# Kernel optimization log

Hardware: AMD Instinct MI355X
Metric: run time of the kernel (lower is better)

## Reference

```python
import jax, jax.numpy as jnp
import numpy as np

STRIDE = (2, 2)
PADDING = (1, 1)
DILATION = (1, 1)
KERNEL = (3, 3)


def _out_hw(h_in, w_in):
    h_out = (h_in + 2 * PADDING[0] - DILATION[0] * (KERNEL[0] - 1) - 1) // STRIDE[0] + 1
    w_out = (w_in + 2 * PADDING[1] - DILATION[1] * (KERNEL[1] - 1) - 1) // STRIDE[1] + 1
    return h_out, w_out


def _stride_permutation(h_out, w_out):
    # Single-shot multiplexing row permutation (mirrors _get_stride_permutation).
    s_h, s_w = STRIDE
    if s_h == 1 and s_w == 1:
        return np.arange(h_out * w_out)
    perm = []
    for si in range(s_h):
        for sj in range(s_w):
            for i in range((h_out + s_h - 1) // s_h):
                ai = i * s_h + si
                if ai >= h_out:
                    continue
                for j in range((w_out + s_w - 1) // s_w):
                    aj = j * s_w + sj
                    if aj >= w_out:
                        continue
                    perm.append(ai * w_out + aj)
    return np.asarray(perm, dtype=np.int32)


def setup_inputs() -> dict:
    key = jax.random.key(0)
    kx, kw, kb = jax.random.split(key, 3)
    x = jax.random.normal(kx, (16, 256, 64, 64), dtype=jnp.float32)
    weight = jax.random.normal(kw, (256, 256, 3, 3), dtype=jnp.float32)
    bias = jax.random.normal(kb, (256,), dtype=jnp.float32)
    return {"x": x, "weight": weight, "bias": bias}


def reference(x, weight, bias):
    # Toeplitz matrix-vector product == grouped strided conv.
    out = jax.lax.conv_general_dilated(
        x, weight,
        window_strides=STRIDE,
        padding=[(PADDING[0], PADDING[0]), (PADDING[1], PADDING[1])],
        rhs_dilation=DILATION,
        dimension_numbers=("NCHW", "OIHW", "NCHW"),
        feature_group_count=1,
    )  # [B, Cout, h_out, w_out]
    b, c, h_out, w_out = out.shape
    perm = jnp.asarray(_stride_permutation(h_out, w_out))
    flat = out.reshape(b, c, h_out * w_out)
    # permuted[new_idx] = flat[perm[new_idx]] (single-shot stride multiplexing)
    permuted = flat[:, :, perm]
    return permuted + bias[None, :, None]
```

## Files before the change

kernel.cpp:

```cpp
#include <hip/hip_runtime.h>
#include <cstdint>

typedef __attribute__((ext_vector_type(8))) __bf16 bf16x8;
typedef __attribute__((ext_vector_type(4))) float f32x4;
typedef __attribute__((ext_vector_type(4))) uint32_t u32x4;

#define NB   16
#define CIN  256
#define COUT 256
#define HP   66
#define WP   66
#define KTOT 2304
#define XPB  (HP*WP*256)
#define XPAD_ELEMS (NB*XPB)

__device__ __forceinline__ uint16_t f2bf(float f) {
  uint32_t u = __builtin_bit_cast(uint32_t, f);
  u = (u + 0x7FFFu + ((u >> 16) & 1u)) >> 16;
  return (uint16_t)u;
}

__global__ void prep_kernel(const float* __restrict__ x, const float* __restrict__ w,
                            uint16_t* __restrict__ xpad, uint16_t* __restrict__ bw) {
  const int bid = blockIdx.x;
  const int tid = threadIdx.x;
  if (bid < 2048) {
    const int lane = tid & 63;
    const int wvi = tid >> 6;
    const int chalf = bid & 1;
    const int h = (bid >> 1) & 63;
    const int b = bid >> 7;
    const int c0 = chalf * 128 + wvi * 32;
    const float* src = x + ((size_t)(b * 256 + c0) * 64 + h) * 64 + lane;
    uint16_t* dst = xpad + ((size_t)(b * HP + h + 1) * WP + lane + 1) * 256 + c0;
    #pragma unroll
    for (int g = 0; g < 4; ++g) {
      u32x4 d;
      #pragma unroll
      for (int k = 0; k < 4; ++k) {
        const float v0 = src[(size_t)(g * 8 + 2 * k + 0) * 4096];
        const float v1 = src[(size_t)(g * 8 + 2 * k + 1) * 4096];
        d[k] = (uint32_t)f2bf(v0) | ((uint32_t)f2bf(v1) << 16);
      }
      *(u32x4*)(dst + g * 8) = d;
    }
  } else if (bid < 3088) {
    const int idx = (bid - 2048) * 256 + tid;
    const int b = idx / 16640;
    const int r = idx - b * 16640;
    uint64_t* base = (uint64_t*)(xpad + (size_t)b * XPB);
    int off;
    if (r < 4224) {
      off = r;
    } else if (r < 8448) {
      off = 274560 + (r - 4224);
    } else if (r < 12544) {
      const int i = r - 8448;
      off = (1 + (i >> 6)) * 4224 + (i & 63);
    } else {
      const int i = r - 12544;
      off = (1 + (i >> 6)) * 4224 + 4160 + (i & 63);
    }
    base[off] = 0;
  } else {
    const int gid = (bid - 3088) * 256 + tid;
    const int co = gid / 288;
    const int r = gid - co * 288;
    const int tap = r >> 5;
    const int ci0 = (r & 31) * 8;
    u32x4 d;
    #pragma unroll
    for (int k = 0; k < 4; ++k) {
      const float v0 = w[((co * 256 + ci0 + 2 * k + 0) * 9) + tap];
      const float v1 = w[((co * 256 + ci0 + 2 * k + 1) * 9) + tap];
      d[k] = (uint32_t)f2bf(v0) | ((uint32_t)f2bf(v1) << 16);
    }
    *(u32x4*)(bw + co * KTOT + tap * 256 + ci0) = d;
  }
}

__device__ __forceinline__ void gl_lds16(const void* g, void* l) {
  __builtin_amdgcn_global_load_lds(
      (__attribute__((address_space(1))) void*)(uintptr_t)g,
      (__attribute__((address_space(3))) void*)(uint32_t)(uintptr_t)l,
      16, 0, 0);
}

__global__ __launch_bounds__(256, 2) void gemm_kernel(
    const uint16_t* __restrict__ xpad, const uint16_t* __restrict__ bw,
    const float* __restrict__ bias, float* __restrict__ out) {
  __shared__ uint16_t lA[2][128 * 64];
  __shared__ uint16_t lB[2][64 * 64];
  const int tid = threadIdx.x;
  const int wv = tid >> 6, lane = tid & 63;
  const int quad = lane >> 4, l15 = lane & 15, l7 = lane & 7;

  const int xcd = blockIdx.x & 7;
  const int grp = blockIdx.x >> 3;
  const int mtile = (xcd << 4) + (grp >> 2);
  const int ntile = grp & 3;
  const int n0 = ntile * 64;
  const int m0 = mtile * 128;
  const int bidx = m0 >> 10;
  const int q0 = m0 & 1023;

  int a_goff[4];
  #pragma unroll
  for (int t = 0; t < 4; ++t) {
    const int slot = t * 256 + tid;
    const int row = slot >> 3;
    const int kc = (slot & 7) ^ (row & 7);
    const int p = q0 + row;
    const int oh = 2 * ((p >> 4) & 15) + ((p >> 9) & 1);
    const int ow = 2 * (p & 15) + ((p >> 8) & 1);
    a_goff[t] = ((bidx * HP + 2 * oh) * WP + 2 * ow) * 256 + kc * 8;
  }
  int b_goff[2];
  #pragma unroll
  for (int t = 0; t < 2; ++t) {
    const int slot = t * 256 + tid;
    const int n = slot >> 3;
    const int kc = (slot & 7) ^ (n & 7);
    b_goff[t] = (n0 + n) * KTOT + kc * 8;
  }

  int aoff[2][2], boff[4][2];
  #pragma unroll
  for (int r = 0; r < 2; ++r)
    #pragma unroll
    for (int s = 0; s < 2; ++s)
      aoff[r][s] = (wv * 32 + r * 16 + l15) * 128 + (((s * 4 + quad) ^ l7) * 16);
  #pragma unroll
  for (int c = 0; c < 4; ++c)
    #pragma unroll
    for (int s = 0; s < 2; ++s)
      boff[c][s] = (c * 16 + l15) * 128 + (((s * 4 + quad) ^ l7) * 16);

  f32x4 acc[2][4];
  #pragma unroll
  for (int r = 0; r < 2; ++r)
    #pragma unroll
    for (int c = 0; c < 4; ++c)
      acc[r][c] = (f32x4){0.f, 0.f, 0.f, 0.f};

  auto stage = [&](int it, int buf) {
    const int tap = it >> 2;
    const int kh = tap / 3, kw = tap - kh * 3;
    const int ci0 = (it & 3) << 6;
    const uint16_t* aptr = xpad + (kh * WP + kw) * 256 + ci0;
    const uint16_t* bptr = bw + tap * 256 + ci0;
    char* la = (char*)&lA[buf][0];
    char* lb = (char*)&lB[buf][0];
    #pragma unroll
    for (int t = 0; t < 4; ++t)
      gl_lds16(aptr + a_goff[t], la + (t * 256 + wv * 64) * 16);
    #pragma unroll
    for (int t = 0; t < 2; ++t)
      gl_lds16(bptr + b_goff[t], lb + (t * 256 + wv * 64) * 16);
  };

  stage(0, 0);
  int buf = 0;
  for (int it = 0; it < 36; ++it) {
    __syncthreads();
    if (it < 35) stage(it + 1, buf ^ 1);
    const char* la = (const char*)&lA[buf][0];
    const char* lb = (const char*)&lB[buf][0];
    #pragma unroll
    for (int s = 0; s < 2; ++s) {
      bf16x8 af[2], bfr[4];
      #pragma unroll
      for (int r = 0; r < 2; ++r) af[r] = *(const bf16x8*)(la + aoff[r][s]);
      #pragma unroll
      for (int c = 0; c < 4; ++c) bfr[c] = *(const bf16x8*)(lb + boff[c][s]);
      #pragma unroll
      for (int r = 0; r < 2; ++r)
        #pragma unroll
        for (int c = 0; c < 4; ++c)
          acc[r][c] = __builtin_amdgcn_mfma_f32_16x16x32_bf16(af[r], bfr[c], acc[r][c], 0, 0, 0);
    }
    buf ^= 1;
  }

  float* obase = out + (size_t)bidx * (COUT * 1024);
  #pragma unroll
  for (int c = 0; c < 4; ++c) {
    const int co = n0 + c * 16 + l15;
    const float bv = bias[co];
    #pragma unroll
    for (int r = 0; r < 2; ++r) {
      const int q = q0 + wv * 32 + r * 16 + quad * 4;
      f32x4 v = acc[r][c];
      v += bv;
      *(f32x4*)(obase + (size_t)co * 1024 + q) = v;
    }
  }
}

extern "C" void kernel_launch(void* const* d_in, const int* in_sizes, int n_in,
                              void* d_out, int out_size, void* d_ws, size_t ws_size,
                              hipStream_t stream) {
  const float* x    = (const float*)d_in[0];
  const float* w    = (const float*)d_in[1];
  const float* bias = (const float*)d_in[2];
  float* out = (float*)d_out;
  uint16_t* xpad = (uint16_t*)d_ws;
  uint16_t* bwq  = xpad + XPAD_ELEMS;

  prep_kernel<<<dim3(3376), dim3(256), 0, stream>>>(x, w, xpad, bwq);
  gemm_kernel<<<dim3(512), dim3(256), 0, stream>>>(xpad, bwq, bias, out);
}
```

Measured before the change: 138.5 us.

## Load A operand directly from global into registers, bypassing LDS

```diff
diff --git a/kernel.cpp b/kernel.cpp
--- a/kernel.cpp
+++ b/kernel.cpp
@@ -89,7 +89,6 @@
 __global__ __launch_bounds__(256, 2) void gemm_kernel(
     const uint16_t* __restrict__ xpad, const uint16_t* __restrict__ bw,
     const float* __restrict__ bias, float* __restrict__ out) {
-  __shared__ uint16_t lA[2][128 * 64];
   __shared__ uint16_t lB[2][64 * 64];
   const int tid = threadIdx.x;
   const int wv = tid >> 6, lane = tid & 63;
@@ -104,17 +103,16 @@
   const int bidx = m0 >> 10;
   const int q0 = m0 & 1023;
 
-  int a_goff[4];
-  #pragma unroll
-  for (int t = 0; t < 4; ++t) {
-    const int slot = t * 256 + tid;
-    const int row = slot >> 3;
-    const int kc = (slot & 7) ^ (row & 7);
-    const int p = q0 + row;
+  int P[2];
+  #pragma unroll
+  for (int r = 0; r < 2; ++r) {
+    const int m = wv * 32 + r * 16 + l15;
+    const int p = q0 + m;
     const int oh = 2 * ((p >> 4) & 15) + ((p >> 9) & 1);
     const int ow = 2 * (p & 15) + ((p >> 8) & 1);
-    a_goff[t] = ((bidx * HP + 2 * oh) * WP + 2 * ow) * 256 + kc * 8;
-  }
+    P[r] = ((bidx * HP + 2 * oh) * WP + 2 * ow) * 256;
+  }
+
   int b_goff[2];
   #pragma unroll
   for (int t = 0; t < 2; ++t) {
@@ -124,12 +122,7 @@
     b_goff[t] = (n0 + n) * KTOT + kc * 8;
   }
 
-  int aoff[2][2], boff[4][2];
-  #pragma unroll
-  for (int r = 0; r < 2; ++r)
-    #pragma unroll
-    for (int s = 0; s < 2; ++s)
-      aoff[r][s] = (wv * 32 + r * 16 + l15) * 128 + (((s * 4 + quad) ^ l7) * 16);
+  int boff[4][2];
   #pragma unroll
   for (int c = 0; c < 4; ++c)
     #pragma unroll
@@ -143,43 +136,54 @@
     for (int c = 0; c < 4; ++c)
       acc[r][c] = (f32x4){0.f, 0.f, 0.f, 0.f};
 
-  auto stage = [&](int it, int buf) {
+  bf16x8 Ar[2][2][2];
+
+  auto stageB = [&](int it, int buf) {
     const int tap = it >> 2;
-    const int kh = tap / 3, kw = tap - kh * 3;
-    const int ci0 = (it & 3) << 6;
-    const uint16_t* aptr = xpad + (kh * WP + kw) * 256 + ci0;
-    const uint16_t* bptr = bw + tap * 256 + ci0;
-    char* la = (char*)&lA[buf][0];
+    const uint16_t* bptr = bw + tap * 256 + ((it & 3) << 6);
     char* lb = (char*)&lB[buf][0];
-    #pragma unroll
-    for (int t = 0; t < 4; ++t)
-      gl_lds16(aptr + a_goff[t], la + (t * 256 + wv * 64) * 16);
     #pragma unroll
     for (int t = 0; t < 2; ++t)
       gl_lds16(bptr + b_goff[t], lb + (t * 256 + wv * 64) * 16);
   };
-
-  stage(0, 0);
-  int buf = 0;
-  for (int it = 0; it < 36; ++it) {
-    __syncthreads();
-    if (it < 35) stage(it + 1, buf ^ 1);
-    const char* la = (const char*)&lA[buf][0];
+  auto loadA = [&](int it, bf16x8 (&dst)[2][2]) {
+    const int tap = it >> 2;
+    const int kh = tap / 3, kw = tap - kh * 3;
+    const int off = (kh * WP + kw) * 256 + ((it & 3) << 6) + quad * 8;
+    #pragma unroll
+    for (int r = 0; r < 2; ++r)
+      #pragma unroll
+      for (int s = 0; s < 2; ++s)
+        dst[r][s] = *(const bf16x8*)(xpad + P[r] + off + s * 32);
+  };
+  auto compute = [&](int buf, bf16x8 (&af)[2][2]) {
     const char* lb = (const char*)&lB[buf][0];
     #pragma unroll
     for (int s = 0; s < 2; ++s) {
-      bf16x8 af[2], bfr[4];
-      #pragma unroll
-      for (int r = 0; r < 2; ++r) af[r] = *(const bf16x8*)(la + aoff[r][s]);
+      bf16x8 bfr[4];
       #pragma unroll
       for (int c = 0; c < 4; ++c) bfr[c] = *(const bf16x8*)(lb + boff[c][s]);
       #pragma unroll
       for (int r = 0; r < 2; ++r)
         #pragma unroll
         for (int c = 0; c < 4; ++c)
-          acc[r][c] = __builtin_amdgcn_mfma_f32_16x16x32_bf16(af[r], bfr[c], acc[r][c], 0, 0, 0);
-    }
-    buf ^= 1;
+          acc[r][c] = __builtin_amdgcn_mfma_f32_16x16x32_bf16(af[r][s], bfr[c], acc[r][c], 0, 0, 0);
+    }
+  };
+
+  stageB(0, 0);
+  loadA(0, Ar[0]);
+  for (int it = 0; it < 36; it += 2) {
+    __syncthreads();
+    stageB(it + 1, 1);
+    loadA(it + 1, Ar[1]);
+    compute(0, Ar[0]);
+    __syncthreads();
+    if (it + 2 < 36) {
+      stageB(it + 2, 0);
+      loadA(it + 2, Ar[0]);
+    }
+    compute(1, Ar[1]);
   }
 
   float* obase = out + (size_t)bidx * (COUT * 1024);
```

New measurement: 156.0 us. +12.6%, slower.

## Triple-buffer LDS staging with explicit vmcnt waits and tap-major K order

Applied to the files above, without the earlier changes.

```diff
diff --git a/kernel.cpp b/kernel.cpp
--- a/kernel.cpp
+++ b/kernel.cpp
@@ -89,8 +89,8 @@
 __global__ __launch_bounds__(256, 2) void gemm_kernel(
     const uint16_t* __restrict__ xpad, const uint16_t* __restrict__ bw,
     const float* __restrict__ bias, float* __restrict__ out) {
-  __shared__ uint16_t lA[2][128 * 64];
-  __shared__ uint16_t lB[2][64 * 64];
+  __shared__ uint16_t lA[3][128 * 64];
+  __shared__ uint16_t lB[3][64 * 64];
   const int tid = threadIdx.x;
   const int wv = tid >> 6, lane = tid & 63;
   const int quad = lane >> 4, l15 = lane & 15, l7 = lane & 7;
@@ -143,14 +143,15 @@
     for (int c = 0; c < 4; ++c)
       acc[r][c] = (f32x4){0.f, 0.f, 0.f, 0.f};
 
-  auto stage = [&](int it, int buf) {
-    const int tap = it >> 2;
-    const int kh = tap / 3, kw = tap - kh * 3;
-    const int ci0 = (it & 3) << 6;
-    const uint16_t* aptr = xpad + (kh * WP + kw) * 256 + ci0;
-    const uint16_t* bptr = bw + tap * 256 + ci0;
-    char* la = (char*)&lA[buf][0];
-    char* lb = (char*)&lB[buf][0];
+  auto stageK = [&](int it, int slot) {
+    const int cc = (it * 57) >> 9;
+    const int tap = it - cc * 9;
+    const int kh = (tap * 11) >> 5;
+    const int kw = tap - kh * 3;
+    const uint16_t* aptr = xpad + (kh * WP + kw) * 256 + cc * 64;
+    const uint16_t* bptr = bw + tap * 256 + cc * 64;
+    char* la = (char*)&lA[slot][0];
+    char* lb = (char*)&lB[slot][0];
     #pragma unroll
     for (int t = 0; t < 4; ++t)
       gl_lds16(aptr + a_goff[t], la + (t * 256 + wv * 64) * 16);
@@ -158,14 +159,9 @@
     for (int t = 0; t < 2; ++t)
       gl_lds16(bptr + b_goff[t], lb + (t * 256 + wv * 64) * 16);
   };
-
-  stage(0, 0);
-  int buf = 0;
-  for (int it = 0; it < 36; ++it) {
-    __syncthreads();
-    if (it < 35) stage(it + 1, buf ^ 1);
-    const char* la = (const char*)&lA[buf][0];
-    const char* lb = (const char*)&lB[buf][0];
+  auto compute = [&](int slot) {
+    const char* la = (const char*)&lA[slot][0];
+    const char* lb = (const char*)&lB[slot][0];
     #pragma unroll
     for (int s = 0; s < 2; ++s) {
       bf16x8 af[2], bfr[4];
@@ -179,7 +175,18 @@
         for (int c = 0; c < 4; ++c)
           acc[r][c] = __builtin_amdgcn_mfma_f32_16x16x32_bf16(af[r], bfr[c], acc[r][c], 0, 0, 0);
     }
-    buf ^= 1;
+  };
+
+  stageK(0, 0);
+  stageK(1, 1);
+  for (int it = 0; it < 36; ++it) {
+    if (it < 35)
+      asm volatile("s_waitcnt vmcnt(6) lgkmcnt(0)" ::: "memory");
+    else
+      asm volatile("s_waitcnt vmcnt(0) lgkmcnt(0)" ::: "memory");
+    asm volatile("s_barrier" ::: "memory");
+    if (it + 2 < 36) stageK(it + 2, (it + 2) % 3);
+    compute(it % 3);
   }
 
   float* obase = out + (size_t)bidx * (COUT * 1024);
```

Measured after the change: 141.7 us. 2.3% more time.
